# Kernel tuning notes

Hardware: AMD Instinct MI355X
Metric: run time of the kernel (lower is better)

Reference implementation:

```python
import jax, jax.numpy as jnp
import numpy as np

QMAX = 127.0

def setup_inputs() -> dict:
    key = jax.random.key(0)
    kx, kw, ks = jax.random.split(key, 3)
    B, S, D_IN, D_OUT = 4, 2048, 4096, 4096
    x = jax.random.normal(kx, (B, S, D_IN), dtype=jnp.float16)
    # int8 weight buffer, same distribution as torch.randint(-127, 127)
    weight = jax.random.randint(kw, (D_OUT, D_IN), -127, 127, dtype=jnp.int32).astype(jnp.int8)
    # per-output-channel weight scales (fp16 buffer); small positive values
    weight_scales = (jax.random.uniform(ks, (D_OUT,), dtype=jnp.float32) * 0.01 + 1e-4).astype(jnp.float16)
    return {"x": x, "weight": weight, "weight_scales": weight_scales}

def reference(x, weight, weight_scales):
    # x: [B, S, D_in] fp16; weight: [D_out, D_in] int8; weight_scales: [D_out] fp16
    x32 = x.astype(jnp.float32)
    # dynamic per-token absmax quantization: scale = absmax / 127
    absmax = jnp.max(jnp.abs(x32), axis=-1, keepdims=True)      # [B, S, 1]
    x_scales = jnp.maximum(absmax / QMAX, 1e-8)
    q = jnp.round(x32 / x_scales)                                # in [-127, 127]
    q = jnp.clip(q, -QMAX, QMAX).astype(jnp.int8)
    # int8 GEMM accumulated in int32 (cupy.matmul on int32 in the original)
    y = jnp.einsum('bsk,nk->bsn', q.astype(jnp.int32), weight.astype(jnp.int32),
                   preferred_element_type=jnp.int32)             # [B, S, D_out]
    # dequant: per-token activation scale * per-channel weight scale
    y = y.astype(jnp.float32) * x_scales * weight_scales.astype(jnp.float32)[None, None, :]
    return y.astype(jnp.float16)
```

## Files before the change

### kernel.cpp

```cpp
#include <hip/hip_runtime.h>
#include <stdint.h>

typedef int int32x4  __attribute__((ext_vector_type(4)));
typedef int int32x16 __attribute__((ext_vector_type(16)));

constexpr int K_DIM = 4096;
constexpr int N_DIM = 4096;
constexpr float QMAXF = 127.0f;

__global__ __launch_bounds__(256) void quant_rows(const float* __restrict__ x,
                                                  int8_t* __restrict__ q,
                                                  float* __restrict__ scales) {
    const int row = blockIdx.x;
    const int tid = threadIdx.x;
    const size_t base = (size_t)row * K_DIM;

    const float4* xv = reinterpret_cast<const float4*>(x + base);
    float4 v[4];
#pragma unroll
    for (int i = 0; i < 4; ++i) v[i] = xv[tid + 256 * i];

    float m = 0.0f;
#pragma unroll
    for (int i = 0; i < 4; ++i)
        m = fmaxf(m, fmaxf(fmaxf(fabsf(v[i].x), fabsf(v[i].y)),
                           fmaxf(fabsf(v[i].z), fabsf(v[i].w))));
#pragma unroll
    for (int off = 32; off > 0; off >>= 1) m = fmaxf(m, __shfl_xor(m, off));

    __shared__ float wmax[4];
    if ((tid & 63) == 0) wmax[tid >> 6] = m;
    __syncthreads();
    const float am = fmaxf(fmaxf(wmax[0], wmax[1]), fmaxf(wmax[2], wmax[3]));
    const float scale = fmaxf(am * (1.0f / 127.0f), 1e-8f);
    if (tid == 0) scales[row] = scale;
    const float inv = 1.0f / scale;

    int* qw = reinterpret_cast<int*>(q + base);
#pragma unroll
    for (int i = 0; i < 4; ++i) {
        float f0 = fminf(QMAXF, fmaxf(-QMAXF, rintf(v[i].x * inv)));
        float f1 = fminf(QMAXF, fmaxf(-QMAXF, rintf(v[i].y * inv)));
        float f2 = fminf(QMAXF, fmaxf(-QMAXF, rintf(v[i].z * inv)));
        float f3 = fminf(QMAXF, fmaxf(-QMAXF, rintf(v[i].w * inv)));
        int b0 = ((int)f0) & 255, b1 = ((int)f1) & 255;
        int b2 = ((int)f2) & 255, b3 = ((int)f3) & 255;
        qw[tid + 256 * i] = b0 | (b1 << 8) | (b2 << 16) | (b3 << 24);
    }
}

__global__ __launch_bounds__(256) void pack_w(const int* __restrict__ w,
                                              int8_t* __restrict__ w8) {
    const int idx = blockIdx.x * 256 + threadIdx.x;
    const int4 v = reinterpret_cast<const int4*>(w)[idx];
    int packed = (v.x & 255) | ((v.y & 255) << 8) | ((v.z & 255) << 16) | ((v.w & 255) << 24);
    reinterpret_cast<int*>(w8)[idx] = packed;
}

constexpr int BM = 256, BN = 256, BKB = 128;
constexpr int NT = K_DIM / BKB;

#define GLL(src, dst)                                                          \
    __builtin_amdgcn_global_load_lds(                                          \
        (const __attribute__((address_space(1))) unsigned int*)(src),          \
        (__attribute__((address_space(3))) unsigned int*)(dst), 16, 0, 0)

#define MFMA32(a, b, c) __builtin_amdgcn_mfma_i32_32x32x32_i8((a), (b), (c), 0, 0, 0)

#define MFMA4(ACC, AF, BF)                                                     \
    {                                                                          \
        __builtin_amdgcn_s_setprio(1);                                         \
        ACC = MFMA32(AF[0], BF[0], ACC);                                       \
        ACC = MFMA32(AF[1], BF[1], ACC);                                       \
        ACC = MFMA32(AF[2], BF[2], ACC);                                       \
        ACC = MFMA32(AF[3], BF[3], ACC);                                       \
        __builtin_amdgcn_s_setprio(0);                                         \
    }

#define LDFRAG(DST, P, OFF)                                                    \
    DST[0] = *(const int32x4*)((P) + (OFF) + sl0b);                            \
    DST[1] = *(const int32x4*)((P) + (OFF) + (sl0b ^ 32));                     \
    DST[2] = *(const int32x4*)((P) + (OFF) + 16384 + sl0b);                    \
    DST[3] = *(const int32x4*)((P) + (OFF) + 16384 + (sl0b ^ 32));

__global__ __launch_bounds__(512, 2) void w8a8_gemm256(
        const int8_t* __restrict__ A, const int8_t* __restrict__ B,
        const float* __restrict__ asc, const float* __restrict__ wsc,
        float* __restrict__ C, int M) {
    extern __shared__ int8_t lds[];

    const int tid  = threadIdx.x;
    const int lane = tid & 63;
    const int wave = tid >> 6;

    const int nwg = gridDim.x;
    const int bid = blockIdx.x;
    const int swz = (bid & 7) * (nwg >> 3) + (bid >> 3);
    const int NB  = N_DIM / BN;
    const int brow = (swz / NB) * BM;
    const int bcol = (swz % NB) * BN;

    const int wm = wave >> 2;
    const int wn = wave & 3;
    const int l31 = lane & 31;
    const int lh  = lane >> 5;

    const int rowch = wave * 16 + (lane >> 2);
    const int g     = ((lane & 3) ^ ((lane >> 3) & 3)) * 16;
    const int8_t* gA = A + (size_t)(brow + rowch) * K_DIM + g;
    const int8_t* gB = B + (size_t)(bcol + rowch) * K_DIM + g;
    const int segb = wave * 1024;

    const int q4   = (l31 >> 1) & 3;
    const int sl0b = (lh ^ q4) * 16;
    const int baseA = (wm * 128 + l31) * 64;
    const int baseB = (wn * 64  + l31) * 64;

    int32x16 acc[4][2];
#pragma unroll
    for (int i = 0; i < 4; ++i)
#pragma unroll
        for (int j = 0; j < 2; ++j)
#pragma unroll
            for (int e = 0; e < 16; ++e) acc[i][j][e] = 0;

#pragma unroll
    for (int c = 0; c < 4; ++c) {
        const size_t cg = (size_t)(c & 1) * 128 * K_DIM + (c >> 1) * 64;
        GLL(gA + cg, lds + c * 8192 + segb);
        GLL(gB + cg, lds + 65536 + c * 8192 + segb);
    }
    asm volatile("s_waitcnt vmcnt(0)" ::: "memory");
    __builtin_amdgcn_s_barrier();

    int32x4 af[2][4], bf[2][4];

    for (int t = 0; t < NT; ++t) {
        const int8_t* Ab = lds + (t & 1) * 32768 + baseA;
        const int8_t* Bb = lds + 65536 + (t & 1) * 32768 + baseB;
        int8_t* dA = lds + ((t + 1) & 1) * 32768;
        int8_t* dB = lds + 65536 + ((t + 1) & 1) * 32768;
        const bool pf = (t + 1 < NT);
        const size_t kk = (size_t)(t + 1) * BKB;

        __builtin_amdgcn_s_barrier();
        if (pf) {
#pragma unroll
            for (int c = 0; c < 4; ++c) {
                const size_t cg = (size_t)(c & 1) * 128 * K_DIM + (c >> 1) * 64;
                GLL(gA + kk + cg, dA + c * 8192 + segb);
            }
            asm volatile("s_waitcnt vmcnt(4)" ::: "memory");
        } else {
            asm volatile("s_waitcnt vmcnt(0)" ::: "memory");
        }
        __builtin_amdgcn_s_barrier();

        LDFRAG(af[0], Ab, 0);
        LDFRAG(bf[0], Bb, 0);

        LDFRAG(bf[1], Bb, 2048);
        MFMA4(acc[0][0], af[0], bf[0]);

        LDFRAG(af[1], Ab, 2048);
        MFMA4(acc[0][1], af[0], bf[1]);

        LDFRAG(af[0], Ab, 4096);
        MFMA4(acc[1][0], af[1], bf[0]);

        MFMA4(acc[1][1], af[1], bf[1]);

        LDFRAG(af[1], Ab, 6144);
        MFMA4(acc[2][0], af[0], bf[0]);

        if (pf) {
#pragma unroll
            for (int c = 0; c < 4; ++c) {
                const size_t cg = (size_t)(c & 1) * 128 * K_DIM + (c >> 1) * 64;
                GLL(gB + kk + cg, dB + c * 8192 + segb);
            }
        }
        MFMA4(acc[2][1], af[0], bf[1]);

        MFMA4(acc[3][0], af[1], bf[0]);
        MFMA4(acc[3][1], af[1], bf[1]);
    }

#pragma unroll
    for (int ni = 0; ni < 2; ++ni) {
        const int col = bcol + wn * 64 + ni * 32 + l31;
        const float ws = wsc[col];
#pragma unroll
        for (int mi = 0; mi < 4; ++mi) {
            const int rowb = brow + wm * 128 + mi * 32 + 4 * lh;
#pragma unroll
            for (int r = 0; r < 16; ++r) {
                const int row = rowb + (r & 3) + 8 * (r >> 2);
                float o = (float)acc[mi][ni][r] * asc[row] * ws;
                o = (float)(_Float16)o;
                C[(size_t)row * N_DIM + col] = o;
            }
        }
    }
}

extern "C" void kernel_launch(void* const* d_in, const int* in_sizes, int n_in,
                              void* d_out, int out_size, void* d_ws, size_t ws_size,
                              hipStream_t stream) {
    const float* x   = (const float*)d_in[0];
    const int*   w   = (const int*)d_in[1];
    const float* wsc = (const float*)d_in[2];
    float* out = (float*)d_out;

    const int K = K_DIM;
    const int M = in_sizes[0] / K;
    const int N = N_DIM;

    int8_t* q   = (int8_t*)d_ws;
    int8_t* w8  = (int8_t*)d_ws + (size_t)M * K;
    float*  asc = (float*)((char*)d_ws + (size_t)M * K + (size_t)N * K);

    quant_rows<<<M, 256, 0, stream>>>(x, q, asc);
    pack_w<<<(N * (K / 4)) / 256, 256, 0, stream>>>(w, w8);
    const int grid = (M / BM) * (N / BN);
    w8a8_gemm256<<<grid, 512, 131072, stream>>>(q, w8, asc, wsc, out, M);
}
```

Measured before the change: 194.2 us.

## Restructure LDS tile layout into K-sliced chunks with contiguous fragment reads

Changes how the int8 A/B tiles are staged in LDS: each global-to-LDS load now brings 32-byte k-slices of all 256 rows into separate 8 KB chunks, instead of swizzled 64-byte row halves. Fragment reads become plain contiguous offsets with no XOR swizzle, which simplifies address arithmetic and gives fully linear lane access. The risk is LDS bank conflicts, since the swizzle is removed. Global loads also now cover only 32 contiguous bytes per row per instruction, which may reduce coalescing efficiency.

```diff
diff --git a/kernel.cpp b/kernel.cpp
--- a/kernel.cpp
+++ b/kernel.cpp
@@ -78,10 +78,10 @@
     }
 
 #define LDFRAG(DST, P, OFF)                                                    \
-    DST[0] = *(const int32x4*)((P) + (OFF) + sl0b);                            \
-    DST[1] = *(const int32x4*)((P) + (OFF) + (sl0b ^ 32));                     \
-    DST[2] = *(const int32x4*)((P) + (OFF) + 16384 + sl0b);                    \
-    DST[3] = *(const int32x4*)((P) + (OFF) + 16384 + (sl0b ^ 32));
+    DST[0] = *(const int32x4*)((P) + (OFF));                                   \
+    DST[1] = *(const int32x4*)((P) + (OFF) + 8192);                            \
+    DST[2] = *(const int32x4*)((P) + (OFF) + 16384);                           \
+    DST[3] = *(const int32x4*)((P) + (OFF) + 24576);
 
 __global__ __launch_bounds__(512, 2) void w8a8_gemm256(
         const int8_t* __restrict__ A, const int8_t* __restrict__ B,
@@ -105,16 +105,15 @@
     const int l31 = lane & 31;
     const int lh  = lane >> 5;
 
-    const int rowch = wave * 16 + (lane >> 2);
-    const int g     = ((lane & 3) ^ ((lane >> 3) & 3)) * 16;
-    const int8_t* gA = A + (size_t)(brow + rowch) * K_DIM + g;
-    const int8_t* gB = B + (size_t)(bcol + rowch) * K_DIM + g;
-    const int segb = wave * 1024;
-
-    const int q4   = (l31 >> 1) & 3;
-    const int sl0b = (lh ^ q4) * 16;
-    const int baseA = (wm * 128 + l31) * 64;
-    const int baseB = (wn * 64  + l31) * 64;
+    const int rowch = wave * 32 + (lane >> 1);
+    const int g16   = (lane & 1) * 16;
+    const int8_t* gA = A + (size_t)(brow + rowch) * K_DIM + g16;
+    const int8_t* gB = B + (size_t)(bcol + rowch) * K_DIM + g16;
+    const int segb  = wave * 1024;
+
+    const int laneoff = l31 * 32 + lh * 16;
+    const int aoff = wm * 4096 + laneoff;
+    const int boff = wn * 2048 + laneoff;
 
     int32x16 acc[4][2];
 #pragma unroll
@@ -126,9 +125,8 @@
 
 #pragma unroll
     for (int c = 0; c < 4; ++c) {
-        const size_t cg = (size_t)(c & 1) * 128 * K_DIM + (c >> 1) * 64;
-        GLL(gA + cg, lds + c * 8192 + segb);
-        GLL(gB + cg, lds + 65536 + c * 8192 + segb);
+        GLL(gA + c * 32, lds + c * 8192 + segb);
+        GLL(gB + c * 32, lds + 65536 + c * 8192 + segb);
     }
     asm volatile("s_waitcnt vmcnt(0)" ::: "memory");
     __builtin_amdgcn_s_barrier();
@@ -136,20 +134,18 @@
     int32x4 af[2][4], bf[2][4];
 
     for (int t = 0; t < NT; ++t) {
-        const int8_t* Ab = lds + (t & 1) * 32768 + baseA;
-        const int8_t* Bb = lds + 65536 + (t & 1) * 32768 + baseB;
+        const int8_t* Ab = lds + (t & 1) * 32768 + aoff;
+        const int8_t* Bb = lds + 65536 + (t & 1) * 32768 + boff;
         int8_t* dA = lds + ((t + 1) & 1) * 32768;
         int8_t* dB = lds + 65536 + ((t + 1) & 1) * 32768;
         const bool pf = (t + 1 < NT);
-        const size_t kk = (size_t)(t + 1) * BKB;
+        const int kk = (t + 1) * BKB;
 
         __builtin_amdgcn_s_barrier();
         if (pf) {
 #pragma unroll
-            for (int c = 0; c < 4; ++c) {
-                const size_t cg = (size_t)(c & 1) * 128 * K_DIM + (c >> 1) * 64;
-                GLL(gA + kk + cg, dA + c * 8192 + segb);
-            }
+            for (int c = 0; c < 4; ++c)
+                GLL(gA + kk + c * 32, dA + c * 8192 + segb);
             asm volatile("s_waitcnt vmcnt(4)" ::: "memory");
         } else {
             asm volatile("s_waitcnt vmcnt(0)" ::: "memory");
@@ -159,26 +155,24 @@
         LDFRAG(af[0], Ab, 0);
         LDFRAG(bf[0], Bb, 0);
 
-        LDFRAG(bf[1], Bb, 2048);
+        LDFRAG(bf[1], Bb, 1024);
         MFMA4(acc[0][0], af[0], bf[0]);
 
-        LDFRAG(af[1], Ab, 2048);
+        LDFRAG(af[1], Ab, 1024);
         MFMA4(acc[0][1], af[0], bf[1]);
 
-        LDFRAG(af[0], Ab, 4096);
+        LDFRAG(af[0], Ab, 2048);
         MFMA4(acc[1][0], af[1], bf[0]);
 
         MFMA4(acc[1][1], af[1], bf[1]);
 
-        LDFRAG(af[1], Ab, 6144);
+        LDFRAG(af[1], Ab, 3072);
         MFMA4(acc[2][0], af[0], bf[0]);
 
         if (pf) {
 #pragma unroll
-            for (int c = 0; c < 4; ++c) {
-                const size_t cg = (size_t)(c & 1) * 128 * K_DIM + (c >> 1) * 64;
-                GLL(gB + kk + cg, dB + c * 8192 + segb);
-            }
+            for (int c = 0; c < 4; ++c)
+                GLL(gB + kk + c * 32, dB + c * 8192 + segb);
         }
         MFMA4(acc[2][1], af[0], bf[1]);
 
```

Measured after the change: 206.7 us. 1.06x slower.
